# Optimization experiments

Measured on AMD Instinct MI355X. Metric: run time of the kernel, lower is better.

The kernel has to match this reference:

```python
import jax, jax.numpy as jnp
import numpy as np

B, N, D = 4, 2048, 512      # batch, seq, dim_in
DK = DV = 512               # dim_k == dim_v (required by fc input width)
NH = 8
HK = DK // NH               # per-head dk == dv == 64
SCALE = 1.0 / np.sqrt(HK)
LN_EPS = 1e-5


def setup_inputs() -> dict:
    key = jax.random.key(0)
    ks = jax.random.split(key, 8)
    s = 0.02
    return {
        "x": jax.random.normal(ks[0], (B, N, D), dtype=jnp.float32),
        "Wq": jax.random.normal(ks[1], (D, DK), dtype=jnp.float32) * s,
        "Wk": jax.random.normal(ks[2], (D, DK), dtype=jnp.float32) * s,
        "Wv": jax.random.normal(ks[3], (D, DV), dtype=jnp.float32) * s,
        "Wf": jax.random.normal(ks[4], (2 * DK, D), dtype=jnp.float32) * s,
        "bf": jnp.zeros((D,), dtype=jnp.float32),
        "gamma": jnp.ones((D,), dtype=jnp.float32),
        "beta": jnp.zeros((D,), dtype=jnp.float32),
    }


def reference(x, Wq, Wk, Wv, Wf, bf, gamma, beta):
    b, n, _ = x.shape
    # projections -> [b, nh, n, hk]; q_c/q_f etc. are identical in the source,
    # so compute once.
    def proj(W):
        return jnp.einsum('bnd,dk->bnk', x, W).reshape(b, n, NH, -1).transpose(0, 2, 1, 3)
    q, k, v = proj(Wq), proj(Wk), proj(Wv)

    # conventional branch: softmax over n x n scores
    dist_c = jax.nn.softmax(jnp.einsum('bhqd,bhkd->bhqk', q, k) * SCALE, axis=-1)
    att_c = jnp.einsum('bhqk,bhkd->bhqd', dist_c, v)          # [b,nh,n,hk]
    att_c = att_c.transpose(0, 2, 1, 3).reshape(b, n, DV)

    # feature branch: softmax over dk x dk scores (linear-complexity variant)
    dist_f = jax.nn.softmax(jnp.einsum('bhnk,bhnq->bhkq', k, q) * SCALE, axis=-1)
    att_f = jnp.einsum('bhnd,bhdq->bhnq', v, dist_f)           # [b,nh,n,hk]
    att_f = att_f.transpose(0, 2, 1, 3).reshape(b, n, DV)

    att = jnp.concatenate([att_c, att_f], axis=2)              # [b,n,2*dk]
    out = jax.nn.relu(att @ Wf + bf)                           # dropout=eval (identity)
    out = out + x
    mu = jnp.mean(out, axis=-1, keepdims=True)
    var = jnp.var(out, axis=-1, keepdims=True)
    out = (out - mu) * jax.lax.rsqrt(var + LN_EPS) * gamma + beta
    return out
```

## Files before the change

kernel.cpp:

```cpp
#include <hip/hip_runtime.h>
#include <math.h>
#include <stdint.h>

#define B_   4
#define N_   2048
#define D_   512
#define DK_  512
#define NH_  8
#define HK_  64
#define LN_EPS_ 1e-5f
#define QS_  0.18033688011112042f

typedef unsigned short u16;
typedef __attribute__((ext_vector_type(8))) short short8;
typedef __attribute__((ext_vector_type(4))) float f32x4;
typedef __attribute__((ext_vector_type(8))) unsigned short u16x8;

__device__ __forceinline__ u16 f2bf(float x) {
    uint32_t u = __builtin_bit_cast(uint32_t, x);
    return (u16)((u + 0x7fffu + ((u >> 16) & 1u)) >> 16);
}
__device__ __forceinline__ u16 f2bf_fast(float x) {
    return (u16)((__builtin_bit_cast(uint32_t, x) + 0x8000u) >> 16);
}
__device__ __forceinline__ float b2f(u16 v) {
    return __builtin_bit_cast(float, (uint32_t)v << 16);
}
__device__ __forceinline__ uint32_t cvtpk_bf16(float lo, float hi) {
    uint32_t r;
    asm("v_cvt_pk_bf16_f32 %0, %1, %2" : "=v"(r) : "v"(lo), "v"(hi));
    return r;
}
__device__ __forceinline__ float exp2f_fast(float x) {
    return __builtin_amdgcn_exp2f(x);
}

__device__ __forceinline__ void gload16(const void* g, void* l) {
    __builtin_amdgcn_global_load_lds(
        reinterpret_cast<const __attribute__((address_space(1))) void*>(
            reinterpret_cast<uintptr_t>(g)),
        reinterpret_cast<__attribute__((address_space(3))) void*>(
            static_cast<uint32_t>(reinterpret_cast<uintptr_t>(l))),
        16, 0, 0);
}

__global__ __launch_bounds__(256) void prep_kernel(
    const float* __restrict__ x, const float* __restrict__ Wq,
    const float* __restrict__ Wk, const float* __restrict__ Wv,
    const float* __restrict__ Wf, u16* __restrict__ xb,
    u16* __restrict__ wqkvT, u16* __restrict__ wfT)
{
    __shared__ float t[32][33];
    const int bid = blockIdx.x, tid = threadIdx.x;
    if (bid < 2048) {
        const int i = (bid * 256 + tid) * 8;
        const float4 a = *reinterpret_cast<const float4*>(&x[i]);
        const float4 b = *reinterpret_cast<const float4*>(&x[i + 4]);
        u16x8 o;
        o[0] = f2bf(a.x); o[1] = f2bf(a.y); o[2] = f2bf(a.z); o[3] = f2bf(a.w);
        o[4] = f2bf(b.x); o[5] = f2bf(b.y); o[6] = f2bf(b.z); o[7] = f2bf(b.w);
        *reinterpret_cast<u16x8*>(&xb[i]) = o;
        return;
    }
    const float* W;
    u16* dst;
    int K, Nc, nt, kt;
    if (bid < 2816) {
        const int z = (bid - 2048) >> 8, rem = (bid - 2048) & 255;
        W = z == 0 ? Wq : (z == 1 ? Wk : Wv);
        dst = wqkvT + (size_t)z * 512 * 512;
        K = 512; Nc = 512;
        nt = (rem & 15) * 32; kt = (rem >> 4) * 32;
    } else {
        const int rem = bid - 2816;
        W = Wf; dst = wfT; K = 1024; Nc = 512;
        nt = (rem & 15) * 32; kt = (rem >> 4) * 32;
    }
    {
        const int r = tid >> 3, c0 = (tid & 7) * 4;
        const float4 v = *reinterpret_cast<const float4*>(
            &W[(size_t)(kt + r) * Nc + nt + c0]);
        t[r][c0] = v.x; t[r][c0 + 1] = v.y; t[r][c0 + 2] = v.z; t[r][c0 + 3] = v.w;
    }
    __syncthreads();
    {
        const int nidx = tid >> 3, kc = (tid & 7) * 4;
        u16 o[4];
        #pragma unroll
        for (int j = 0; j < 4; ++j) o[j] = f2bf(t[kc + j][nidx]);
        *reinterpret_cast<ushort4*>(&dst[(size_t)(nt + nidx) * K + kt + kc]) =
            make_ushort4(o[0], o[1], o[2], o[3]);
    }
}

template<int BM, int BN, int MODE>
__global__ __launch_bounds__(256) void gemm_bf16(
    const u16* __restrict__ A, const u16* __restrict__ Bt,
    u16* __restrict__ qb, u16* __restrict__ kb,
    u16* __restrict__ vb, u16* __restrict__ vt, int M, int Nc, int K,
    const float* __restrict__ bias, const float* __restrict__ resid)
{
    constexpr int MI = BM / 32, NI = BN / 32;
    constexpr int AL = BM / 32, BL = BN / 32;
    __shared__ u16 As[BM * 64];
    __shared__ u16 Bs[BN * 64];
    const int tid = threadIdx.x;
    const int lane = tid & 63, wave = tid >> 6;
    const int wm = wave >> 1, wn = wave & 1;
    const int l15 = lane & 15, lg = lane >> 4;

    const int nwg = gridDim.x;
    const int bid = ((int)blockIdx.x & 7) * (nwg >> 3) + ((int)blockIdx.x >> 3);
    const int ntiles = Nc / BN;
    const int nt = (bid % ntiles) * BN;
    const int mt = (bid / ntiles) * BM;

    f32x4 acc[MI][NI] = {};

    for (int kt = 0; kt < K; kt += 64) {
        __syncthreads();
        #pragma unroll
        for (int i = 0; i < AL; ++i) {
            const int ob = (wave * AL + i) * 1024;
            const int o = ob + lane * 16;
            const int row = o >> 7;
            const int inner = (o & 127) ^ ((row & 7) << 4);
            gload16((const char*)A + ((size_t)(mt + row) * K + kt) * 2 + inner,
                    (char*)As + ob);
        }
        #pragma unroll
        for (int i = 0; i < BL; ++i) {
            const int ob = (wave * BL + i) * 1024;
            const int o = ob + lane * 16;
            const int row = o >> 7;
            const int inner = (o & 127) ^ ((row & 7) << 4);
            gload16((const char*)Bt + ((size_t)(nt + row) * K + kt) * 2 + inner,
                    (char*)Bs + ob);
        }
        __syncthreads();
        #pragma unroll
        for (int ks = 0; ks < 2; ++ks) {
            const int kb2 = ks * 32 + lg * 8;
            short8 af[MI], bfr[NI];
            #pragma unroll
            for (int mi = 0; mi < MI; ++mi) {
                const int r = wm * (BM / 2) + mi * 16 + l15;
                af[mi] = *reinterpret_cast<const short8*>(
                    &As[r * 64 + (kb2 ^ ((r & 7) << 3))]);
            }
            #pragma unroll
            for (int ni = 0; ni < NI; ++ni) {
                const int r = wn * (BN / 2) + ni * 16 + l15;
                bfr[ni] = *reinterpret_cast<const short8*>(
                    &Bs[r * 64 + (kb2 ^ ((r & 7) << 3))]);
            }
            #pragma unroll
            for (int mi = 0; mi < MI; ++mi)
                #pragma unroll
                for (int ni = 0; ni < NI; ++ni)
                    acc[mi][ni] = __builtin_amdgcn_mfma_f32_16x16x32_bf16(
                        af[mi], bfr[ni], acc[mi][ni], 0, 0, 0);
        }
    }

    #pragma unroll
    for (int mi = 0; mi < MI; ++mi) {
        #pragma unroll
        for (int ni = 0; ni < NI; ++ni) {
            const int col = nt + wn * (BN / 2) + ni * 16 + l15;
            const int row0 = mt + wm * (BM / 2) + mi * 16 + lg * 4;
            if (MODE == 1) {
                if (col < 512) {
                    #pragma unroll
                    for (int jj = 0; jj < 4; ++jj)
                        qb[(size_t)(row0 + jj) * 512 + col] =
                            f2bf(acc[mi][ni][jj] * QS_);
                } else if (col < 1024) {
                    #pragma unroll
                    for (int jj = 0; jj < 4; ++jj)
                        kb[(size_t)(row0 + jj) * 512 + col - 512] =
                            f2bf(acc[mi][ni][jj]);
                } else {
                    const int dfull = col - 1024;
                    const int hh = dfull >> 6, dd = dfull & 63;
                    const int bb = row0 >> 11, nn = row0 & 2047;
                    u16 o4[4];
                    #pragma unroll
                    for (int jj = 0; jj < 4; ++jj) {
                        o4[jj] = f2bf(acc[mi][ni][jj]);
                        vb[(size_t)(row0 + jj) * 512 + dfull] = o4[jj];
                    }
                    *reinterpret_cast<ushort4*>(
                        &vt[(((size_t)(bb * NH_ + hh)) * HK_ + dd) * N_ + nn]) =
                        make_ushort4(o4[0], o4[1], o4[2], o4[3]);
                }
            } else {
                #pragma unroll
                for (int jj = 0; jj < 4; ++jj) {
                    const size_t row = (size_t)(row0 + jj);
                    float v = acc[mi][ni][jj];
                    v += bias[col];
                    v = fmaxf(v, 0.0f);
                    v += resid[row * Nc + col];
                    qb[row * Nc + col] = f2bf(v);
                }
            }
        }
    }
}

__global__ __launch_bounds__(256) void gemm_fc_kernel(
    const u16* __restrict__ A, const u16* __restrict__ Bt,
    u16* __restrict__ C, const float* __restrict__ bias,
    const float* __restrict__ resid)
{
    __shared__ u16 As0[64 * 64], As1[64 * 64];
    __shared__ u16 Bs0[128 * 64], Bs1[128 * 64];
    const int tid = threadIdx.x;
    const int lane = tid & 63, wave = tid >> 6;
    const int wm = wave >> 1, wn = wave & 1;
    const int l15 = lane & 15, lg = lane >> 4;
    const int bid = ((int)blockIdx.x & 7) * 64 + ((int)blockIdx.x >> 3);
    const int nt = (bid & 3) * 128;
    const int mt = (bid >> 2) * 64;

    f32x4 acc[2][4] = {};

#define FC_STAGE(kt, AS, BS) do {                                              \
    _Pragma("unroll")                                                          \
    for (int i_ = 0; i_ < 2; ++i_) {                                           \
        const int ob_ = (wave * 2 + i_) * 1024;                                \
        const int o_ = ob_ + lane * 16;                                        \
        const int row_ = o_ >> 7;                                              \
        const int inner_ = (o_ & 127) ^ ((row_ & 7) << 4);                     \
        gload16((const char*)A + ((size_t)(mt + row_) * 1024 + (kt) * 64) * 2  \
                    + inner_, (char*)(AS) + ob_);                              \
    }                                                                          \
    _Pragma("unroll")                                                          \
    for (int i_ = 0; i_ < 4; ++i_) {                                           \
        const int ob_ = (wave * 4 + i_) * 1024;                                \
        const int o_ = ob_ + lane * 16;                                        \
        const int row_ = o_ >> 7;                                              \
        const int inner_ = (o_ & 127) ^ ((row_ & 7) << 4);                     \
        gload16((const char*)Bt + ((size_t)(nt + row_) * 1024 + (kt) * 64) * 2 \
                    + inner_, (char*)(BS) + ob_);                              \
    }                                                                          \
} while (0)

#define FC_COMP(AS, BS) do {                                                   \
    _Pragma("unroll")                                                          \
    for (int ks = 0; ks < 2; ++ks) {                                           \
        const int kb2 = ks * 32 + lg * 8;                                      \
        short8 af[2], bfr[4];                                                  \
        _Pragma("unroll")                                                      \
        for (int mi = 0; mi < 2; ++mi) {                                       \
            const int r = wm * 32 + mi * 16 + l15;                             \
            af[mi] = *reinterpret_cast<const short8*>(                         \
                &(AS)[r * 64 + (kb2 ^ ((r & 7) << 3))]);                       \
        }                                                                      \
        _Pragma("unroll")                                                      \
        for (int ni = 0; ni < 4; ++ni) {                                       \
            const int r = wn * 64 + ni * 16 + l15;                             \
            bfr[ni] = *reinterpret_cast<const short8*>(                        \
                &(BS)[r * 64 + (kb2 ^ ((r & 7) << 3))]);                       \
        }                                                                      \
        _Pragma("unroll")                                                      \
        for (int mi = 0; mi < 2; ++mi)                                         \
            _Pragma("unroll")                                                  \
            for (int ni = 0; ni < 4; ++ni)                                     \
                acc[mi][ni] = __builtin_amdgcn_mfma_f32_16x16x32_bf16(         \
                    af[mi], bfr[ni], acc[mi][ni], 0, 0, 0);                    \
    }                                                                          \
} while (0)

    FC_STAGE(0, As0, Bs0);
    __syncthreads();
    #pragma unroll 1
    for (int kt = 0; kt < 16; kt += 2) {
        FC_STAGE(kt + 1, As1, Bs1);
        FC_COMP(As0, Bs0);
        __syncthreads();
        if (kt + 2 < 16) FC_STAGE(kt + 2, As0, Bs0);
        FC_COMP(As1, Bs1);
        __syncthreads();
    }
#undef FC_STAGE
#undef FC_COMP

    #pragma unroll
    for (int mi = 0; mi < 2; ++mi) {
        #pragma unroll
        for (int ni = 0; ni < 4; ++ni) {
            const int col = nt + wn * 64 + ni * 16 + l15;
            const int row0 = mt + wm * 32 + mi * 16 + lg * 4;
            #pragma unroll
            for (int jj = 0; jj < 4; ++jj) {
                const size_t row = (size_t)(row0 + jj);
                float v = acc[mi][ni][jj];
                v += bias[col];
                v = fmaxf(v, 0.0f);
                v += resid[row * 512 + col];
                C[row * 512 + col] = f2bf(v);
            }
        }
    }
}

__global__ __launch_bounds__(256) void flash_featS_kernel(
    const u16* __restrict__ Qb, const u16* __restrict__ Kb,
    const u16* __restrict__ Vt, u16* __restrict__ att,
    float* __restrict__ partials)
{
    __shared__ u16 sh[24576];
    const int tid = threadIdx.x;
    const int lane = tid & 63, wave = tid >> 6;
    const int l15 = lane & 15, lg = lane >> 4;

    if ((int)blockIdx.x >= 512) {
        u16* KsT = sh;
        u16* QsT = sh + 4096;
        const int fid = (int)blockIdx.x - 512;
        const int ns = fid & 7, h = (fid >> 3) & 7, b = fid >> 6;
        const size_t hbase = (size_t)b * N_ * DK_ + (size_t)h * HK_;

        f32x4 acc[4] = {};
        for (int c = 0; c < 4; ++c) {
            const int n0 = ns * 256 + c * 64;
            __syncthreads();
            #pragma unroll
            for (int it = 0; it < 2; ++it) {
                const int idx = tid + it * 256;
                const int n = idx >> 3, d0 = (idx & 7) * 8;
                const u16x8 kv = *reinterpret_cast<const u16x8*>(
                    &Kb[hbase + (size_t)(n0 + n) * DK_ + d0]);
                const u16x8 qv = *reinterpret_cast<const u16x8*>(
                    &Qb[hbase + (size_t)(n0 + n) * DK_ + d0]);
                #pragma unroll
                for (int j = 0; j < 8; ++j) {
                    const int r = d0 + j;
                    const int cidx = n ^ ((r & 7) << 3);
                    KsT[r * 64 + cidx] = kv[j];
                    QsT[r * 64 + cidx] = qv[j];
                }
            }
            __syncthreads();
            #pragma unroll
            for (int ks = 0; ks < 2; ++ks) {
                const int kb2 = ks * 32 + lg * 8;
                const int ar = wave * 16 + l15;
                const short8 aK = *reinterpret_cast<const short8*>(
                    &KsT[ar * 64 + (kb2 ^ ((ar & 7) << 3))]);
                #pragma unroll
                for (int ni = 0; ni < 4; ++ni) {
                    const int br = ni * 16 + l15;
                    const short8 bQ = *reinterpret_cast<const short8*>(
                        &QsT[br * 64 + (kb2 ^ ((br & 7) << 3))]);
                    acc[ni] = __builtin_amdgcn_mfma_f32_16x16x32_bf16(
                        aK, bQ, acc[ni], 0, 0, 0);
                }
            }
        }
        const int bh = b * NH_ + h;
        #pragma unroll
        for (int ni = 0; ni < 4; ++ni)
            #pragma unroll
            for (int jj = 0; jj < 4; ++jj) {
                const int row = wave * 16 + lg * 4 + jj;
                partials[(((size_t)ns * 32 + bh) * 64 + row) * 64 + ni * 16 + l15] =
                    acc[ni][jj];
            }
        return;
    }

    u16* kb0 = sh;
    u16* kb1 = sh + 4096;
    u16* vb0 = sh + 8192;
    u16* vb1 = sh + 12288;
    u16* Ps  = sh + 16384;
    const int lbid = (((int)blockIdx.x & 7) << 6) + ((int)blockIdx.x >> 3);
    const int qt = lbid & 15, h = (lbid >> 4) & 7, b = lbid >> 7;

    short8 aq[2][2];
    #pragma unroll
    for (int qs = 0; qs < 2; ++qs) {
        const int qrow = qt * 128 + qs * 64 + wave * 16 + l15;
        const u16* qp = Qb + ((size_t)(b * N_ + qrow)) * DK_ + h * HK_ + lg * 8;
        aq[qs][0] = *reinterpret_cast<const short8*>(qp);
        aq[qs][1] = *reinterpret_cast<const short8*>(qp + 32);
    }
    short8 ones;
    #pragma unroll
    for (int i = 0; i < 8; ++i) ones[i] = (short)0x3F80;

    const u16* Kbase = Kb + (size_t)b * N_ * DK_ + (size_t)h * HK_;
    const u16* Vbase = Vt + ((size_t)(b * NH_ + h)) * HK_ * N_;
    unsigned long long* Ps64 = reinterpret_cast<unsigned long long*>(Ps);

    f32x4 o[2][5] = {};
    float m_[2] = {-1e30f, -1e30f};
    f32x4 SA[2][4], SB[2][4];

    const int ob0 = wave * 1024, oo0 = ob0 + lane * 16;
    const int row0s = oo0 >> 7;
    const int in0 = (oo0 & 127) ^ ((row0s & 7) << 4);

#define STAGE_K(ktile, KBUF) do {                                              \
    gload16((const char*)Kbase +                                               \
                ((size_t)((ktile) * 64 + row0s) * DK_) * 2 + in0,              \
            (char*)(KBUF) + ob0);                                              \
    gload16((const char*)Kbase +                                               \
                ((size_t)((ktile) * 64 + 32 + row0s) * DK_) * 2 + in0,         \
            (char*)(KBUF) + 4096 + ob0);                                       \
} while (0)

#define STAGE_V(ktile, VBUF) do {                                              \
    gload16((const char*)Vbase +                                               \
                ((size_t)row0s * N_ + (ktile) * 64) * 2 + in0,                 \
            (char*)(VBUF) + ob0);                                              \
    gload16((const char*)Vbase +                                               \
                ((size_t)(32 + row0s) * N_ + (ktile) * 64) * 2 + in0,          \
            (char*)(VBUF) + 4096 + ob0);                                       \
} while (0)

#define QK_STEP(S, KBUF) do {                                                  \
    _Pragma("unroll")                                                          \
    for (int qs = 0; qs < 2; ++qs)                                             \
        _Pragma("unroll")                                                      \
        for (int t = 0; t < 4; ++t)                                            \
            S[qs][t] = (f32x4){0.0f, 0.0f, 0.0f, 0.0f};                        \
    __builtin_amdgcn_s_setprio(1);                                             \
    _Pragma("unroll")                                                          \
    for (int ks = 0; ks < 2; ++ks) {                                           \
        const int kb2 = ks * 32 + lg * 8;                                      \
        _Pragma("unroll")                                                      \
        for (int t = 0; t < 4; ++t) {                                          \
            const int r = t * 16 + l15;                                        \
            const short8 bk = *reinterpret_cast<const short8*>(                \
                &(KBUF)[r * 64 + (kb2 ^ ((r & 7) << 3))]);                     \
            S[0][t] = __builtin_amdgcn_mfma_f32_16x16x32_bf16(                 \
                bk, aq[0][ks], S[0][t], 0, 0, 0);                              \
            S[1][t] = __builtin_amdgcn_mfma_f32_16x16x32_bf16(                 \
                bk, aq[1][ks], S[1][t], 0, 0, 0);                              \
        }                                                                      \
    }                                                                          \
    __builtin_amdgcn_s_setprio(0);                                             \
} while (0)

#define SMPV_STEP(S, VBUF) do {                                                \
    float rmax[2], cm;                                                         \
    _Pragma("unroll")                                                          \
    for (int qs = 0; qs < 2; ++qs) {                                           \
        float a0 = fmaxf(fmaxf(S[qs][0][0], S[qs][0][1]),                      \
                         fmaxf(S[qs][0][2], S[qs][0][3]));                     \
        float a1 = fmaxf(fmaxf(S[qs][1][0], S[qs][1][1]),                      \
                         fmaxf(S[qs][1][2], S[qs][1][3]));                     \
        float a2 = fmaxf(fmaxf(S[qs][2][0], S[qs][2][1]),                      \
                         fmaxf(S[qs][2][2], S[qs][2][3]));                     \
        float a3 = fmaxf(fmaxf(S[qs][3][0], S[qs][3][1]),                      \
                         fmaxf(S[qs][3][2], S[qs][3][3]));                     \
        rmax[qs] = fmaxf(fmaxf(a0, a1), fmaxf(a2, a3));                        \
    }                                                                          \
    cm = fmaxf(rmax[0] - m_[0], rmax[1] - m_[1]);                              \
    if (__any(cm > 8.0f)) {                                                    \
        _Pragma("unroll")                                                      \
        for (int qs = 0; qs < 2; ++qs) {                                       \
            float rm = rmax[qs];                                               \
            rm = fmaxf(rm, __shfl_xor(rm, 16));                                \
            rm = fmaxf(rm, __shfl_xor(rm, 32));                                \
            const float newm = fmaxf(m_[qs], rm);                              \
            const float fac = exp2f_fast(m_[qs] - newm);                       \
            m_[qs] = newm;                                                     \
            float facq[4];                                                     \
            _Pragma("unroll")                                                  \
            for (int jj = 0; jj < 4; ++jj)                                     \
                facq[jj] = __shfl(fac, lg * 4 + jj);                           \
            _Pragma("unroll")                                                  \
            for (int t = 0; t < 5; ++t)                                        \
                _Pragma("unroll")                                              \
                for (int jj = 0; jj < 4; ++jj)                                 \
                    o[qs][t][jj] *= facq[jj];                                  \
        }                                                                      \
    }                                                                          \
    _Pragma("unroll")                                                          \
    for (int qs = 0; qs < 2; ++qs) {                                           \
        const int prow = qs * 64 + wave * 16 + l15;                            \
        const int pb64 = prow * 16;                                            \
        const int sw1 = (prow & 7) << 1;                                       \
        _Pragma("unroll")                                                      \
        for (int t = 0; t < 4; ++t) {                                          \
            const float p0 = exp2f_fast(S[qs][t][0] - m_[qs]);                 \
            const float p1 = exp2f_fast(S[qs][t][1] - m_[qs]);                 \
            const float p2 = exp2f_fast(S[qs][t][2] - m_[qs]);                 \
            const float p3 = exp2f_fast(S[qs][t][3] - m_[qs]);                 \
            const uint32_t lo = cvtpk_bf16(p0, p1);                            \
            const uint32_t hi = cvtpk_bf16(p2, p3);                            \
            Ps64[pb64 + ((t * 4 + lg) ^ sw1)] =                                \
                (unsigned long long)lo | ((unsigned long long)hi << 32);       \
        }                                                                      \
    }                                                                          \
    __builtin_amdgcn_s_setprio(1);                                             \
    _Pragma("unroll")                                                          \
    for (int ks = 0; ks < 2; ++ks) {                                           \
        const int kb2 = ks * 32 + lg * 8;                                      \
        const int pr0 = wave * 16 + l15;                                       \
        const int pr1 = 64 + pr0;                                              \
        const short8 ap0 = *reinterpret_cast<const short8*>(                   \
            &Ps[pr0 * 64 + (kb2 ^ ((pr0 & 7) << 3))]);                         \
        const short8 ap1 = *reinterpret_cast<const short8*>(                   \
            &Ps[pr1 * 64 + (kb2 ^ ((pr1 & 7) << 3))]);                         \
        _Pragma("unroll")                                                      \
        for (int t = 0; t < 4; ++t) {                                          \
            const int dr = t * 16 + l15;                                       \
            const short8 bv = *reinterpret_cast<const short8*>(                \
                &(VBUF)[dr * 64 + (kb2 ^ ((dr & 7) << 3))]);                   \
            o[0][t] = __builtin_amdgcn_mfma_f32_16x16x32_bf16(                 \
                ap0, bv, o[0][t], 0, 0, 0);                                    \
            o[1][t] = __builtin_amdgcn_mfma_f32_16x16x32_bf16(                 \
                ap1, bv, o[1][t], 0, 0, 0);                                    \
        }                                                                      \
        o[0][4] = __builtin_amdgcn_mfma_f32_16x16x32_bf16(                     \
            ap0, ones, o[0][4], 0, 0, 0);                                      \
        o[1][4] = __builtin_amdgcn_mfma_f32_16x16x32_bf16(                     \
            ap1, ones, o[1][4], 0, 0, 0);                                      \
    }                                                                          \
    __builtin_amdgcn_s_setprio(0);                                             \
} while (0)

    STAGE_K(0, kb0);
    STAGE_K(1, kb1);
    STAGE_V(0, vb0);
    __syncthreads();
    QK_STEP(SA, kb0);

    #pragma unroll 1
    for (int t2 = 0; t2 < 30; t2 += 2) {
        __syncthreads();
        STAGE_K(t2 + 2, kb0);
        STAGE_V(t2 + 1, vb1);
        QK_STEP(SB, kb1);
        SMPV_STEP(SA, vb0);
        __syncthreads();
        STAGE_K(t2 + 3, kb1);
        STAGE_V(t2 + 2, vb0);
        QK_STEP(SA, kb0);
        SMPV_STEP(SB, vb1);
    }
    __syncthreads();
    STAGE_V(31, vb1);
    QK_STEP(SB, kb1);
    SMPV_STEP(SA, vb0);
    __syncthreads();
    SMPV_STEP(SB, vb1);

#undef STAGE_K
#undef STAGE_V
#undef QK_STEP
#undef SMPV_STEP

    #pragma unroll
    for (int qs = 0; qs < 2; ++qs)
        #pragma unroll
        for (int jj = 0; jj < 4; ++jj) {
            const float inv = 1.0f / o[qs][4][jj];
            const size_t row = (size_t)b * N_ + qt * 128 + qs * 64 + wave * 16 + lg * 4 + jj;
            #pragma unroll
            for (int t = 0; t < 4; ++t)
                att[row * (2 * DK_) + h * HK_ + t * 16 + l15] =
                    f2bf_fast(o[qs][t][jj] * inv);
        }
}

__global__ __launch_bounds__(256) void featSM_kernel(
    const float* __restrict__ partials, u16* __restrict__ distfT)
{
    const int bh = blockIdx.x, rg = blockIdx.y, tid = threadIdx.x;
    const int r = rg * 16 + (tid >> 4);
    const int tl = tid & 15;
    float v[4] = {0.0f, 0.0f, 0.0f, 0.0f};
    for (int s = 0; s < 8; ++s) {
        const float4 a = *reinterpret_cast<const float4*>(
            &partials[(((size_t)s * 32 + bh) * 64 + r) * 64 + tl * 4]);
        v[0] += a.x; v[1] += a.y; v[2] += a.z; v[3] += a.w;
    }
    float m = fmaxf(fmaxf(v[0], v[1]), fmaxf(v[2], v[3]));
    m = fmaxf(m, __shfl_xor(m, 1));
    m = fmaxf(m, __shfl_xor(m, 2));
    m = fmaxf(m, __shfl_xor(m, 4));
    m = fmaxf(m, __shfl_xor(m, 8));
    float sum = 0.0f;
    #pragma unroll
    for (int j = 0; j < 4; ++j) { v[j] = exp2f_fast(v[j] - m); sum += v[j]; }
    sum += __shfl_xor(sum, 1);
    sum += __shfl_xor(sum, 2);
    sum += __shfl_xor(sum, 4);
    sum += __shfl_xor(sum, 8);
    const float inv = 1.0f / sum;
    #pragma unroll
    for (int j = 0; j < 4; ++j)
        distfT[(size_t)bh * 4096 + (tl * 4 + j) * 64 + r] = f2bf_fast(v[j] * inv);
}

__global__ __launch_bounds__(256) void featAV_mfma(
    const u16* __restrict__ V, const u16* __restrict__ distfT,
    u16* __restrict__ att)
{
    __shared__ u16 Bs[64 * 64];
    __shared__ u16 As[64 * 64];
    const int tid = threadIdx.x;
    const int lane = tid & 63, wave = tid >> 6;
    const int l15 = lane & 15, lg = lane >> 4;
    const int ns = blockIdx.x, h = blockIdx.y, b = blockIdx.z;
    const int bh = b * NH_ + h;
    const int n0 = ns * 64;

    #pragma unroll
    for (int it = 0; it < 2; ++it) {
        const int idx = tid + it * 256;
        const int r = idx >> 3, c0 = (idx & 7) * 8;
        const u16x8 dv = *reinterpret_cast<const u16x8*>(
            &distfT[(size_t)bh * 4096 + r * 64 + c0]);
        *reinterpret_cast<u16x8*>(&Bs[r * 64 + (c0 ^ ((r & 7) << 3))]) = dv;
    }
    #pragma unroll
    for (int i = 0; i < 2; ++i) {
        const int ob = (wave * 2 + i) * 1024;
        const int o_ = ob + lane * 16;
        const int row = o_ >> 7;
        const int inner = (o_ & 127) ^ ((row & 7) << 4);
        gload16((const char*)V + ((size_t)(b * N_ + n0 + row) * DK_ + h * HK_) * 2 + inner,
                (char*)As + ob);
    }
    __syncthreads();
    f32x4 acc[4] = {};
    #pragma unroll
    for (int ks = 0; ks < 2; ++ks) {
        const int kb2 = ks * 32 + lg * 8;
        const int ar = wave * 16 + l15;
        const short8 av = *reinterpret_cast<const short8*>(
            &As[ar * 64 + (kb2 ^ ((ar & 7) << 3))]);
        #pragma unroll
        for (int ni = 0; ni < 4; ++ni) {
            const int br = ni * 16 + l15;
            const short8 bd = *reinterpret_cast<const short8*>(
                &Bs[br * 64 + (kb2 ^ ((br & 7) << 3))]);
            acc[ni] = __builtin_amdgcn_mfma_f32_16x16x32_bf16(av, bd, acc[ni], 0, 0, 0);
        }
    }
    #pragma unroll
    for (int ni = 0; ni < 4; ++ni)
        #pragma unroll
        for (int jj = 0; jj < 4; ++jj)
            att[((size_t)b * N_ + n0 + wave * 16 + lg * 4 + jj) * (2 * DK_)
                + 512 + h * HK_ + ni * 16 + l15] = f2bf_fast(acc[ni][jj]);
}

__global__ __launch_bounds__(256) void ln_kernel(
    const u16* __restrict__ fc, const float* __restrict__ gamma,
    const float* __restrict__ beta, float* __restrict__ out)
{
    const int row = blockIdx.x * 4 + (threadIdx.x >> 6);
    const int lane = threadIdx.x & 63;
    const int c = lane * 8;
    const u16x8 v = *reinterpret_cast<const u16x8*>(&fc[(size_t)row * D_ + c]);
    float f[8];
    float s = 0.0f, sq = 0.0f;
    #pragma unroll
    for (int j = 0; j < 8; ++j) {
        f[j] = b2f(v[j]);
        s += f[j];
        sq = fmaf(f[j], f[j], sq);
    }
    #pragma unroll
    for (int off = 32; off >= 1; off >>= 1) {
        s  += __shfl_xor(s, off);
        sq += __shfl_xor(sq, off);
    }
    const float mu = s * (1.0f / D_);
    const float var = sq * (1.0f / D_) - mu * mu;
    const float rstd = rsqrtf(var + LN_EPS_);
    const float4 g0 = *reinterpret_cast<const float4*>(&gamma[c]);
    const float4 g1 = *reinterpret_cast<const float4*>(&gamma[c + 4]);
    const float4 b0 = *reinterpret_cast<const float4*>(&beta[c]);
    const float4 b1 = *reinterpret_cast<const float4*>(&beta[c + 4]);
    const float gg[8] = {g0.x, g0.y, g0.z, g0.w, g1.x, g1.y, g1.z, g1.w};
    const float bb[8] = {b0.x, b0.y, b0.z, b0.w, b1.x, b1.y, b1.z, b1.w};
    float4 o0, o1;
    o0.x = (f[0] - mu) * rstd * gg[0] + bb[0];
    o0.y = (f[1] - mu) * rstd * gg[1] + bb[1];
    o0.z = (f[2] - mu) * rstd * gg[2] + bb[2];
    o0.w = (f[3] - mu) * rstd * gg[3] + bb[3];
    o1.x = (f[4] - mu) * rstd * gg[4] + bb[4];
    o1.y = (f[5] - mu) * rstd * gg[5] + bb[5];
    o1.z = (f[6] - mu) * rstd * gg[6] + bb[6];
    o1.w = (f[7] - mu) * rstd * gg[7] + bb[7];
    *reinterpret_cast<float4*>(&out[(size_t)row * D_ + c]) = o0;
    *reinterpret_cast<float4*>(&out[(size_t)row * D_ + c + 4]) = o1;
}

extern "C" void kernel_launch(void* const* d_in, const int* in_sizes, int n_in,
                              void* d_out, int out_size, void* d_ws, size_t ws_size,
                              hipStream_t stream)
{
    (void)in_sizes; (void)n_in; (void)out_size; (void)ws_size;
    const float* x     = (const float*)d_in[0];
    const float* Wq    = (const float*)d_in[1];
    const float* Wk    = (const float*)d_in[2];
    const float* Wv    = (const float*)d_in[3];
    const float* Wf    = (const float*)d_in[4];
    const float* bf    = (const float*)d_in[5];
    const float* gamma = (const float*)d_in[6];
    const float* beta  = (const float*)d_in[7];
    float* out = (float*)d_out;

    char* w = (char*)d_ws;
    const size_t SZE = (size_t)B_ * N_ * DK_;
    u16* xb     = (u16*)w;   w += SZE * 2;
    u16* wqkvT  = (u16*)w;   w += (size_t)1536 * 512 * 2;
    u16* wfT    = (u16*)w;   w += (size_t)512 * 1024 * 2;
    u16* qb     = (u16*)w;   w += SZE * 2;
    u16* kb     = (u16*)w;   w += SZE * 2;
    u16* vb     = (u16*)w;   w += SZE * 2;
    u16* vt     = (u16*)w;   w += SZE * 2;
    u16* attb   = (u16*)w;   w += SZE * 2 * 2;
    float* partials = (float*)w; w += (size_t)8 * 32 * 4096 * 4;
    u16* distfT = (u16*)w;   w += (size_t)32 * 4096 * 2;
    u16* fcout  = (u16*)w;

    const dim3 blk(256);
    const int M = B_ * N_;

    prep_kernel<<<dim3(3328), blk, 0, stream>>>(x, Wq, Wk, Wv, Wf, xb, wqkvT, wfT);

    gemm_bf16<128, 128, 1><<<dim3(768), blk, 0, stream>>>(
        xb, wqkvT, qb, kb, vb, vt, M, 1536, 512, nullptr, nullptr);

    flash_featS_kernel<<<dim3(768), blk, 0, stream>>>(qb, kb, vt, attb, partials);

    featSM_kernel<<<dim3(32, 4), blk, 0, stream>>>(partials, distfT);
    featAV_mfma<<<dim3(32, NH_, B_), blk, 0, stream>>>(vb, distfT, attb);

    gemm_fc_kernel<<<dim3(512), blk, 0, stream>>>(attb, wfT, fcout, bf, x);

    ln_kernel<<<dim3(2048), blk, 0, stream>>>(fcout, gamma, beta, out);
}
```

Before: 120.6 us.

## Double-buffer QKV projection GEMM with smaller 64x128 tiles and more blocks

Replaces the generic templated GEMM used for the QKV projection with a dedicated kernel. It uses 64x128 tiles instead of 128x128, which doubles the grid to 1536 workgroups, and double-buffers the LDS tiles so the next K-slice's global loads overlap the MFMA compute on the current slice. This should hide global memory latency and improve load balance across CUs. The cost is more LDS per block, lower per-block arithmetic intensity, and more redundant weight reads.

After: 116.3 us (median of 2 runs). 3.6% less time.

```diff
diff --git a/kernel.cpp b/kernel.cpp
--- a/kernel.cpp
+++ b/kernel.cpp
@@ -93,117 +93,113 @@
     }
 }
 
-template<int BM, int BN, int MODE>
-__global__ __launch_bounds__(256) void gemm_bf16(
+__global__ __launch_bounds__(256) void gemm_qkv_kernel(
     const u16* __restrict__ A, const u16* __restrict__ Bt,
     u16* __restrict__ qb, u16* __restrict__ kb,
-    u16* __restrict__ vb, u16* __restrict__ vt, int M, int Nc, int K,
-    const float* __restrict__ bias, const float* __restrict__ resid)
+    u16* __restrict__ vb, u16* __restrict__ vt)
 {
-    constexpr int MI = BM / 32, NI = BN / 32;
-    constexpr int AL = BM / 32, BL = BN / 32;
-    __shared__ u16 As[BM * 64];
-    __shared__ u16 Bs[BN * 64];
+    __shared__ u16 As0[64 * 64], As1[64 * 64];
+    __shared__ u16 Bs0[128 * 64], Bs1[128 * 64];
     const int tid = threadIdx.x;
     const int lane = tid & 63, wave = tid >> 6;
     const int wm = wave >> 1, wn = wave & 1;
     const int l15 = lane & 15, lg = lane >> 4;
-
-    const int nwg = gridDim.x;
-    const int bid = ((int)blockIdx.x & 7) * (nwg >> 3) + ((int)blockIdx.x >> 3);
-    const int ntiles = Nc / BN;
-    const int nt = (bid % ntiles) * BN;
-    const int mt = (bid / ntiles) * BM;
-
-    f32x4 acc[MI][NI] = {};
-
-    for (int kt = 0; kt < K; kt += 64) {
+    const int bid = ((int)blockIdx.x & 7) * 192 + ((int)blockIdx.x >> 3);
+    const int nt = (bid % 12) * 128;
+    const int mt = (bid / 12) * 64;
+
+    f32x4 acc[2][4] = {};
+
+#define QKV_STAGE(kt, AS, BS) do {                                             \
+    _Pragma("unroll")                                                          \
+    for (int i_ = 0; i_ < 2; ++i_) {                                           \
+        const int ob_ = (wave * 2 + i_) * 1024;                                \
+        const int o_ = ob_ + lane * 16;                                        \
+        const int row_ = o_ >> 7;                                              \
+        const int inner_ = (o_ & 127) ^ ((row_ & 7) << 4);                     \
+        gload16((const char*)A + ((size_t)(mt + row_) * 512 + (kt) * 64) * 2   \
+                    + inner_, (char*)(AS) + ob_);                              \
+    }                                                                          \
+    _Pragma("unroll")                                                          \
+    for (int i_ = 0; i_ < 4; ++i_) {                                           \
+        const int ob_ = (wave * 4 + i_) * 1024;                                \
+        const int o_ = ob_ + lane * 16;                                        \
+        const int row_ = o_ >> 7;                                              \
+        const int inner_ = (o_ & 127) ^ ((row_ & 7) << 4);                     \
+        gload16((const char*)Bt + ((size_t)(nt + row_) * 512 + (kt) * 64) * 2  \
+                    + inner_, (char*)(BS) + ob_);                              \
+    }                                                                          \
+} while (0)
+
+#define QKV_COMP(AS, BS) do {                                                  \
+    _Pragma("unroll")                                                          \
+    for (int ks = 0; ks < 2; ++ks) {                                           \
+        const int kb2 = ks * 32 + lg * 8;                                      \
+        short8 af[2], bfr[4];                                                  \
+        _Pragma("unroll")                                                      \
+        for (int mi = 0; mi < 2; ++mi) {                                       \
+            const int r = wm * 32 + mi * 16 + l15;                             \
+            af[mi] = *reinterpret_cast<const short8*>(                         \
+                &(AS)[r * 64 + (kb2 ^ ((r & 7) << 3))]);                       \
+        }                                                                      \
+        _Pragma("unroll")                                                      \
+        for (int ni = 0; ni < 4; ++ni) {                                       \
+            const int r = wn * 64 + ni * 16 + l15;                             \
+            bfr[ni] = *reinterpret_cast<const short8*>(                        \
+                &(BS)[r * 64 + (kb2 ^ ((r & 7) << 3))]);                       \
+        }                                                                      \
+        _Pragma("unroll")                                                      \
+        for (int mi = 0; mi < 2; ++mi)                                         \
+            _Pragma("unroll")                                                  \
+            for (int ni = 0; ni < 4; ++ni)                                     \
+                acc[mi][ni] = __builtin_amdgcn_mfma_f32_16x16x32_bf16(         \
+                    af[mi], bfr[ni], acc[mi][ni], 0, 0, 0);                    \
+    }                                                                          \
+} while (0)
+
+    QKV_STAGE(0, As0, Bs0);
+    __syncthreads();
+    #pragma unroll 1
+    for (int kt = 0; kt < 8; kt += 2) {
+        QKV_STAGE(kt + 1, As1, Bs1);
+        QKV_COMP(As0, Bs0);
         __syncthreads();
+        if (kt + 2 < 8) QKV_STAGE(kt + 2, As0, Bs0);
+        QKV_COMP(As1, Bs1);
+        __syncthreads();
+    }
+#undef QKV_STAGE
+#undef QKV_COMP
+
+    #pragma unroll
+    for (int mi = 0; mi < 2; ++mi) {
         #pragma unroll
-        for (int i = 0; i < AL; ++i) {
-            const int ob = (wave * AL + i) * 1024;
-            const int o = ob + lane * 16;
-            const int row = o >> 7;
-            const int inner = (o & 127) ^ ((row & 7) << 4);
-            gload16((const char*)A + ((size_t)(mt + row) * K + kt) * 2 + inner,
-                    (char*)As + ob);
-        }
-        #pragma unroll
-        for (int i = 0; i < BL; ++i) {
-            const int ob = (wave * BL + i) * 1024;
-            const int o = ob + lane * 16;
-            const int row = o >> 7;
-            const int inner = (o & 127) ^ ((row & 7) << 4);
-            gload16((const char*)Bt + ((size_t)(nt + row) * K + kt) * 2 + inner,
-                    (char*)Bs + ob);
-        }
-        __syncthreads();
-        #pragma unroll
-        for (int ks = 0; ks < 2; ++ks) {
-            const int kb2 = ks * 32 + lg * 8;
-            short8 af[MI], bfr[NI];
-            #pragma unroll
-            for (int mi = 0; mi < MI; ++mi) {
-                const int r = wm * (BM / 2) + mi * 16 + l15;
-                af[mi] = *reinterpret_cast<const short8*>(
-                    &As[r * 64 + (kb2 ^ ((r & 7) << 3))]);
-            }
-            #pragma unroll
-            for (int ni = 0; ni < NI; ++ni) {
-                const int r = wn * (BN / 2) + ni * 16 + l15;
-                bfr[ni] = *reinterpret_cast<const short8*>(
-                    &Bs[r * 64 + (kb2 ^ ((r & 7) << 3))]);
-            }
-            #pragma unroll
-            for (int mi = 0; mi < MI; ++mi)
+        for (int ni = 0; ni < 4; ++ni) {
+            const int col = nt + wn * 64 + ni * 16 + l15;
+            const int row0 = mt + wm * 32 + mi * 16 + lg * 4;
+            if (col < 512) {
                 #pragma unroll
-                for (int ni = 0; ni < NI; ++ni)
-                    acc[mi][ni] = __builtin_amdgcn_mfma_f32_16x16x32_bf16(
-                        af[mi], bfr[ni], acc[mi][ni], 0, 0, 0);
-        }
-    }
-
-    #pragma unroll
-    for (int mi = 0; mi < MI; ++mi) {
-        #pragma unroll
-        for (int ni = 0; ni < NI; ++ni) {
-            const int col = nt + wn * (BN / 2) + ni * 16 + l15;
-            const int row0 = mt + wm * (BM / 2) + mi * 16 + lg * 4;
-            if (MODE == 1) {
-                if (col < 512) {
-                    #pragma unroll
-                    for (int jj = 0; jj < 4; ++jj)
-                        qb[(size_t)(row0 + jj) * 512 + col] =
-                            f2bf(acc[mi][ni][jj] * QS_);
-                } else if (col < 1024) {
-                    #pragma unroll
-                    for (int jj = 0; jj < 4; ++jj)
-                        kb[(size_t)(row0 + jj) * 512 + col - 512] =
-                            f2bf(acc[mi][ni][jj]);
-                } else {
-                    const int dfull = col - 1024;
-                    const int hh = dfull >> 6, dd = dfull & 63;
-                    const int bb = row0 >> 11, nn = row0 & 2047;
-                    u16 o4[4];
-                    #pragma unroll
-                    for (int jj = 0; jj < 4; ++jj) {
-                        o4[jj] = f2bf(acc[mi][ni][jj]);
-                        vb[(size_t)(row0 + jj) * 512 + dfull] = o4[jj];
-                    }
-                    *reinterpret_cast<ushort4*>(
-                        &vt[(((size_t)(bb * NH_ + hh)) * HK_ + dd) * N_ + nn]) =
-                        make_ushort4(o4[0], o4[1], o4[2], o4[3]);
-                }
+                for (int jj = 0; jj < 4; ++jj)
+                    qb[(size_t)(row0 + jj) * 512 + col] =
+                        f2bf(acc[mi][ni][jj] * QS_);
+            } else if (col < 1024) {
+                #pragma unroll
+                for (int jj = 0; jj < 4; ++jj)
+                    kb[(size_t)(row0 + jj) * 512 + col - 512] =
+                        f2bf(acc[mi][ni][jj]);
             } else {
+                const int dfull = col - 1024;
+                const int hh = dfull >> 6, dd = dfull & 63;
+                const int bb = row0 >> 11, nn = row0 & 2047;
+                u16 o4[4];
                 #pragma unroll
                 for (int jj = 0; jj < 4; ++jj) {
-                    const size_t row = (size_t)(row0 + jj);
-                    float v = acc[mi][ni][jj];
-                    v += bias[col];
-                    v = fmaxf(v, 0.0f);
-                    v += resid[row * Nc + col];
-                    qb[row * Nc + col] = f2bf(v);
+                    o4[jj] = f2bf(acc[mi][ni][jj]);
+                    vb[(size_t)(row0 + jj) * 512 + dfull] = o4[jj];
                 }
+                *reinterpret_cast<ushort4*>(
+                    &vt[(((size_t)(bb * NH_ + hh)) * HK_ + dd) * N_ + nn]) =
+                    make_ushort4(o4[0], o4[1], o4[2], o4[3]);
             }
         }
     }
@@ -727,12 +723,10 @@
     u16* fcout  = (u16*)w;
 
     const dim3 blk(256);
-    const int M = B_ * N_;
 
     prep_kernel<<<dim3(3328), blk, 0, stream>>>(x, Wq, Wk, Wv, Wf, xb, wqkvT, wfT);
 
-    gemm_bf16<128, 128, 1><<<dim3(768), blk, 0, stream>>>(
-        xb, wqkvT, qb, kb, vb, vt, M, 1536, 512, nullptr, nullptr);
+    gemm_qkv_kernel<<<dim3(1536), blk, 0, stream>>>(xb, wqkvT, qb, kb, vb, vt);
 
     flash_featS_kernel<<<dim3(768), blk, 0, stream>>>(qb, kb, vt, attb, partials);
 
```
